# Performance work log

Hardware: AMD Instinct MI355X
Metric: run time of the kernel (lower is better)

## Reference

```python
import jax, jax.numpy as jnp
import numpy as np

# Module constants (from source defaults)
RING = 256      # ring_len
D = 128         # slot_dim
IN = 64         # input_dim
SD = max(8, D // 3)  # sensory_dim = 42
K = 2           # gauss_k -> 2K+1 = 5 taps
TAU = 8.0       # gauss_tau
NC = 1000       # num_classes
B, T = 512, 512


def setup_inputs() -> dict:
    key = jax.random.key(0)
    ks = jax.random.split(key, 10)
    g = lambda k, shape, s=0.05: jax.random.normal(k, shape, jnp.float32) * s
    return {
        "x": jax.random.normal(ks[0], (B, T, IN), jnp.float32),
        "theta_ptr": jnp.array([37.0], jnp.float32),
        "w_proj": g(ks[1], (SD, IN)), "b_proj": jnp.zeros((SD,), jnp.float32),
        "w_ih": g(ks[2], (3 * SD, SD)), "w_hh": g(ks[3], (3 * SD, SD)),
        "b_ih": jnp.zeros((3 * SD,), jnp.float32), "b_hh": jnp.zeros((3 * SD,), jnp.float32),
        "w_bridge": g(ks[4], (D, SD)), "b_bridge": jnp.zeros((D,), jnp.float32),
        "w_jump": g(ks[5], (1, D)), "b_jump": jnp.zeros((1,), jnp.float32),
        "w_gate": g(ks[6], (1, D)), "b_gate": jnp.zeros((1,), jnp.float32),
        "w_cls": g(ks[7], (NC, D)), "b_cls": jnp.zeros((NC,), jnp.float32),
    }


def _kernel(ptr):
    """Gaussian soft window around a fractional ring pointer. ptr: [B] float."""
    offs = jnp.arange(-K, K + 1)
    base = jnp.floor(ptr)
    frac = ptr - base                               # [B]
    pos = jnp.mod(base.astype(jnp.int32)[:, None] + offs[None, :], RING)  # [B, 2K+1]
    d = offs.astype(ptr.dtype)[None, :] - frac[:, None]
    w = jax.nn.softmax(-(d * d) / TAU, axis=-1)     # [B, 2K+1]
    return pos, w


def reference(x, theta_ptr, w_proj, b_proj, w_ih, w_hh, b_ih, b_hh,
              w_bridge, b_bridge, w_jump, b_jump, w_gate, b_gate, w_cls, b_cls):
    Bn = x.shape[0]
    bidx = jnp.arange(Bn)
    ring0 = jnp.zeros((Bn, RING, D), x.dtype)
    h0 = jnp.zeros((Bn, SD), x.dtype)
    ptr0 = jnp.broadcast_to(jnp.mod(theta_ptr, float(RING)), (Bn,)).astype(x.dtype)

    def step(carry, xt):
        ring, h, ptr = carry
        # sensory path: Linear -> GRUCell -> bridge
        s = xt @ w_proj.T + b_proj
        gx = s @ w_ih.T + b_ih
        gh = h @ w_hh.T + b_hh
        rg = jax.nn.sigmoid(gx[:, :SD] + gh[:, :SD])
        zg = jax.nn.sigmoid(gx[:, SD:2 * SD] + gh[:, SD:2 * SD])
        ng = jnp.tanh(gx[:, 2 * SD:] + rg * gh[:, 2 * SD:])
        h = (1.0 - zg) * ng + zg * h
        u = jnp.tanh(h @ w_bridge.T + b_bridge)      # write vector [B, D]
        # soft-kernel read at current pointer
        pos, w = _kernel(ptr)
        r = jnp.einsum('bk,bkd->bd', w, ring[bidx[:, None], pos])
        # pointer jump target + gate, circ_lerp along shortest arc
        jump = jax.nn.sigmoid(r @ w_jump.T + b_jump)[:, 0] * RING
        gate = jax.nn.sigmoid(r @ w_gate.T + b_gate)[:, 0]
        delta = jnp.mod(jump - ptr + RING / 2.0, float(RING)) - RING / 2.0  # wrap_delta
        ptr = jnp.mod(ptr + gate * delta, float(RING))                      # circ_lerp
        # soft-kernel write at new pointer
        pos2, w2 = _kernel(ptr)
        ring = ring.at[bidx[:, None], pos2].add(w2[..., None] * u[:, None, :])
        return (ring, h, ptr), None

    (ring, h, ptr), _ = jax.lax.scan(step, (ring0, h0, ptr0), jnp.swapaxes(x, 0, 1))
    pos, w = _kernel(ptr)
    r = jnp.einsum('bk,bkd->bd', w, ring[bidx[:, None], pos])
    return r @ w_cls.T + b_cls
```

## Files before the change

### kernel.cpp

```cpp
#include <hip/hip_runtime.h>
#include <hip/hip_bf16.h>
#include <cstdint>

#define RINGN 256
#define DD    128
#define SDN   42
#define G3N   126
#define INN   64
#define BN    512
#define TN    512
#define NCN   1000
#define HS    44
#define GXS   128
#define BT    (BN * TN)
#define HSLOTS 32

typedef float v2f __attribute__((ext_vector_type(2)));
typedef float4 __attribute__((may_alias)) f4ma;
typedef float2 __attribute__((may_alias)) f2ma;

__device__ __forceinline__ float sigm(float x)    { return 1.0f / (1.0f + __expf(-x)); }
__device__ __forceinline__ float tanhfast(float x){ float e = __expf(2.0f * x); return 1.0f - 2.0f / (e + 1.0f); }
__device__ __forceinline__ float wrap256(float x) { return x - 256.0f * floorf(x * 0.00390625f); }

__device__ __forceinline__ void taps_norm(float p, int* pos, float* w) {
  float base = floorf(p);
  float frac = p - base;
  int ib = (int)base;
  float e[5];
  float s = 0.0f;
#pragma unroll
  for (int k = 0; k < 5; k++) {
    float d = (float)(k - 2) - frac;
    e[k] = __expf(-(d * d) * 0.125f);
    s += e[k];
    pos[k] = (ib + k - 2) & 255;
  }
  float inv = 1.0f / s;
#pragma unroll
  for (int k = 0; k < 5; k++) w[k] = e[k] * inv;
}

template<int C>
__device__ __forceinline__ float dpp_add_step(float x) {
  int t = __builtin_amdgcn_update_dpp(0, __float_as_int(x), C, 0xf, 0xf, true);
  return x + __int_as_float(t);
}
__device__ __forceinline__ float wave_sum64(float x) {
  x = dpp_add_step<0x111>(x);
  x = dpp_add_step<0x112>(x);
  x = dpp_add_step<0x114>(x);
  x = dpp_add_step<0x118>(x);
  x = dpp_add_step<0x142>(x);
  x = dpp_add_step<0x143>(x);
  return __int_as_float(__builtin_amdgcn_readlane(__float_as_int(x), 63));
}

__global__ void prep_kernel(const float* __restrict__ w_ih, const float* __restrict__ w_proj,
                            const float* __restrict__ b_proj, const float* __restrict__ b_ih,
                            float* __restrict__ Wc, float* __restrict__ bc) {
  int idx = blockIdx.x * 256 + threadIdx.x;
  if (idx < G3N * INN) {
    int j = idx / INN, i = idx % INN;
    float a = 0.0f;
    for (int k = 0; k < SDN; k++) a += w_ih[j * SDN + k] * w_proj[k * INN + i];
    Wc[idx] = a;
  }
  if (idx < G3N) {
    float a = b_ih[idx];
    for (int k = 0; k < SDN; k++) a += w_ih[idx * SDN + k] * b_proj[k];
    bc[idx] = a;
  }
}

__global__ __launch_bounds__(256)
void gx_gemm(const float* __restrict__ x, const float* __restrict__ Wc,
             const float* __restrict__ bc, float* __restrict__ gxp) {
  __shared__ __align__(16) float WcS[G3N * INN];
  __shared__ float bcS[G3N + 2];
  __shared__ float tileS[256 * 33];
  const int tid = threadIdx.x;
  const float4* wc4 = (const float4*)Wc;
  float4* wcs4 = (float4*)WcS;
  for (int i = tid; i < G3N * INN / 4; i += 256) wcs4[i] = wc4[i];
  if (tid < G3N) bcS[tid] = bc[tid];
  __syncthreads();

  const size_t row0 = (size_t)blockIdx.x * 256;
  const size_t row = row0 + tid;
  v2f xr[INN / 2];
#pragma unroll
  for (int i = 0; i < INN / 4; i++) {
    float4 v = *reinterpret_cast<const float4*>(&x[row * INN + i * 4]);
    xr[2 * i]     = (v2f){v.x, v.y};
    xr[2 * i + 1] = (v2f){v.z, v.w};
  }

  for (int c0 = 0; c0 < GXS; c0 += 32) {
#pragma unroll
    for (int cc = 0; cc < 32; cc++) {
      int c = c0 + cc;
      float val = 0.0f;
      if (c < G3N) {
        const v2f* w = (const v2f*)&WcS[c * INN];
        v2f acc2 = (v2f){bcS[c], 0.0f};
#pragma unroll
        for (int i = 0; i < INN / 2; i++) acc2 = __builtin_elementwise_fma(w[i], xr[i], acc2);
        val = acc2.x + acc2.y;
      }
      tileS[tid * 33 + cc] = val;
    }
    __syncthreads();
#pragma unroll
    for (int i = 0; i < 8; i++) {
      int f = i * 256 + tid;
      int r = f >> 3;
      int cc4 = (f & 7) * 4;
      float4 v = make_float4(tileS[r * 33 + cc4], tileS[r * 33 + cc4 + 1],
                             tileS[r * 33 + cc4 + 2], tileS[r * 33 + cc4 + 3]);
      *reinterpret_cast<float4*>(&gxp[(row0 + r) * GXS + c0 + cc4]) = v;
    }
    __syncthreads();
  }
}

__global__ __launch_bounds__(192, 1)
void rec3_kernel(const float* __restrict__ gxp,
                 const float* __restrict__ w_hh, const float* __restrict__ b_hh,
                 const float* __restrict__ w_bridge, const float* __restrict__ b_bridge,
                 const float* __restrict__ w_jump, const float* __restrict__ b_jump,
                 const float* __restrict__ w_gate, const float* __restrict__ b_gate,
                 const float* __restrict__ theta,
                 float* __restrict__ hbuf, float* __restrict__ ptrbuf) {
  const int tid = threadIdx.x;
  const int wid = tid >> 6;
  const int lane = tid & 63;
  const int b = blockIdx.x;

  __shared__ float2 JG[RINGN];
  __shared__ __align__(16) float h_ring[HSLOTS * HS];
  __shared__ float ringJ[TN];
  __shared__ float ringG[TN];
  __shared__ int flagH;
  __shared__ int done1;

  if (tid == 0) { flagH = 0; done1 = 0; }
  __syncthreads();

  if (wid == 0) {
    const int jj = (lane < SDN) ? lane : (SDN - 1);

    const v2f* whh2 = (const v2f*)w_hh;
    v2f Whr[21], Whz[21], Whn[21];
#pragma unroll
    for (int k = 0; k < 21; k++) {
      Whr[k] = whh2[jj * 21 + k];
      Whz[k] = whh2[(jj + SDN) * 21 + k];
      Whn[k] = whh2[(jj + 2 * SDN) * 21 + k];
    }
    const float bhr = b_hh[jj], bhz = b_hh[jj + SDN], bhn = b_hh[jj + 2 * SDN];

    v2f hv2[22];
#pragma unroll
    for (int k = 0; k < 22; k++) hv2[k] = (v2f){0.f, 0.f};
    float hprev = 0.0f;

    const float* gxr = gxp + (size_t)b * TN * GXS;
    const int o0 = jj, o1 = SDN + jj, o2 = 2 * SDN + jj;
    float* hb = hbuf + (size_t)b * TN * HS;

    float pA0 = gxr[o0], pA1 = gxr[o1], pA2 = gxr[o2];
    float pB0 = gxr[GXS + o0], pB1 = gxr[GXS + o1], pB2 = gxr[GXS + o2];

    volatile int* fH = &flagH;
    volatile int* fC = &done1;

    auto STEP = [&](int t, float pgx0, float pgx1, float pgx2) {
      if ((t & 7) == 0 && t >= HSLOTS) {
        while (*fC < t - 24) __builtin_amdgcn_s_sleep(1);
      }
      v2f ar = (v2f){bhr, 0.f}, az = (v2f){bhz, 0.f}, an = (v2f){bhn, 0.f};
#pragma unroll
      for (int k = 0; k < 21; k++) {
        v2f h2 = hv2[k];
        ar = __builtin_elementwise_fma(Whr[k], h2, ar);
        az = __builtin_elementwise_fma(Whz[k], h2, az);
        an = __builtin_elementwise_fma(Whn[k], h2, an);
      }
      float ghr = ar.x + ar.y, ghz = az.x + az.y, ghn = an.x + an.y;
      float rgate = sigm(pgx0 + ghr);
      float zg = sigm(pgx1 + ghz);
      float ng = tanhfast(pgx2 + rgate * ghn);
      float hn = (1.0f - zg) * ng + zg * hprev;
      hprev = hn;

      float* slot = &h_ring[(t & (HSLOTS - 1)) * HS];
      if (lane < SDN) {
        slot[lane] = hn;
        hb[(size_t)t * HS + lane] = hn;
      }
      asm volatile("s_waitcnt lgkmcnt(0)" ::: "memory");
      if (lane == 0) *fH = t + 1;
      __builtin_amdgcn_wave_barrier();
      asm volatile("" ::: "memory");

#pragma unroll
      for (int i = 0; i < 11; i++) {
        float4 v = *(const f4ma*)(&slot[i * 4]);
        hv2[2 * i]     = (v2f){v.x, v.y};
        hv2[2 * i + 1] = (v2f){v.z, v.w};
      }
    };

    for (int t = 0; t < TN; t += 2) {
      STEP(t, pA0, pA1, pA2);
      if (t + 2 < TN) {
        const float* g = gxr + (size_t)(t + 2) * GXS;
        pA0 = g[o0]; pA1 = g[o1]; pA2 = g[o2];
      }
      STEP(t + 1, pB0, pB1, pB2);
      if (t + 3 < TN) {
        const float* g = gxr + (size_t)(t + 3) * GXS;
        pB0 = g[o0]; pB1 = g[o1]; pB2 = g[o2];
      }
    }
  } else if (wid == 1) {
    const int r1 = lane + 64;
    const v2f* wb2 = (const v2f*)w_bridge;
    v2f Wb0[21], Wb1[21];
#pragma unroll
    for (int k = 0; k < 21; k++) {
      Wb0[k] = wb2[lane * 21 + k];
      Wb1[k] = wb2[r1 * 21 + k];
    }
    const float bb0 = b_bridge[lane], bb1 = b_bridge[r1];
    const float wj0 = w_jump[lane], wj1 = w_jump[r1];
    const float wg0 = w_gate[lane], wg1 = w_gate[r1];

    volatile int* fH = &flagH;
    volatile int* fC = &done1;
    int seenH = 0;

    for (int t = 0; t < TN; t++) {
      if (seenH <= t) {
        while ((seenH = *fH) <= t) __builtin_amdgcn_s_sleep(1);
      }
      asm volatile("" ::: "memory");
      const float* slot = &h_ring[(t & (HSLOTS - 1)) * HS];
      v2f hw[22];
#pragma unroll
      for (int i = 0; i < 11; i++) {
        float4 v = *(const f4ma*)(&slot[i * 4]);
        hw[2 * i]     = (v2f){v.x, v.y};
        hw[2 * i + 1] = (v2f){v.z, v.w};
      }
      v2f a0 = (v2f){bb0, 0.f}, a1 = (v2f){bb1, 0.f};
#pragma unroll
      for (int k = 0; k < 21; k++) {
        v2f h2 = hw[k];
        a0 = __builtin_elementwise_fma(Wb0[k], h2, a0);
        a1 = __builtin_elementwise_fma(Wb1[k], h2, a1);
      }
      float u0 = tanhfast(a0.x + a0.y);
      float u1 = tanhfast(a1.x + a1.y);

      float pjs = wave_sum64(u0 * wj0 + u1 * wj1);
      float pgs = wave_sum64(u0 * wg0 + u1 * wg1);

      if (lane == 0) { ringJ[t] = pjs; ringG[t] = pgs; }
      asm volatile("s_waitcnt lgkmcnt(0)" ::: "memory");
      if (lane == 0) *fC = t + 1;
    }
  } else {
    for (int i = lane; i < RINGN; i += 64) JG[i] = make_float2(0.f, 0.f);
    __builtin_amdgcn_wave_barrier();
    asm volatile("" ::: "memory");

    const float bj = b_jump[0], bg = b_gate[0];
    float ptr = wrap256(theta[0]);
    float* pb = ptrbuf + (size_t)b * TN;

    float wk[5]; float2 Vk[5];
    {
      int posk[5];
      taps_norm(ptr, posk, wk);
#pragma unroll
      for (int k = 0; k < 5; k++) Vk[k] = JG[posk[k]];
    }
    float pjprev = 0.f, pgprev = 0.f, S2prev = 0.f;
    volatile int* rdy = &done1;
    int seen = 0;

    for (int t = 0; t < TN; t++) {
      float dotJ = 0.f, dotG = 0.f;
#pragma unroll
      for (int k = 0; k < 5; k++) { dotJ += wk[k] * Vk[k].x; dotG += wk[k] * Vk[k].y; }
      float Jv = fmaf(pjprev, S2prev, dotJ);
      float Gv = fmaf(pgprev, S2prev, dotG);
      float jump = 256.0f * sigm(Jv + bj);
      float gate = sigm(Gv + bg);
      float delta = wrap256(jump - ptr + 128.0f) - 128.0f;
      float ptr2 = wrap256(ptr + gate * delta);

      float tbase = floorf(ptr2);
      float frac = ptr2 - tbase;
      int ib = (int)tbase;
      float e2[5], ssum = 0.f; int pos2[5];
#pragma unroll
      for (int k = 0; k < 5; k++) {
        float d = (float)(k - 2) - frac;
        e2[k] = __expf(-(d * d) * 0.125f);
        ssum += e2[k];
        pos2[k] = (ib + k - 2) & 255;
      }
      float inv2 = 1.0f / ssum;
      float2 Vk2[5];
#pragma unroll
      for (int k = 0; k < 5; k++) Vk2[k] = JG[pos2[k]];
      float w2n[5], S2 = 0.f;
#pragma unroll
      for (int k = 0; k < 5; k++) { w2n[k] = e2[k] * inv2; S2 = fmaf(w2n[k], w2n[k], S2); }
      if (lane == 0) pb[t] = ptr2;

      if (seen <= t) {
        while ((seen = *rdy) <= t) __builtin_amdgcn_s_sleep(1);
      }
      asm volatile("" ::: "memory");
      float pjs = ringJ[t];
      float pgs = ringG[t];

      int p2sel = pos2[0]; float w2sel = w2n[0];
#pragma unroll
      for (int k = 1; k < 5; k++) {
        if (lane == k) { p2sel = pos2[k]; w2sel = w2n[k]; }
      }
      if (lane < 5) {
        atomicAdd(&JG[p2sel].x, w2sel * pjs);
        atomicAdd(&JG[p2sel].y, w2sel * pgs);
      }

#pragma unroll
      for (int k = 0; k < 5; k++) { wk[k] = w2n[k]; Vk[k] = Vk2[k]; }
      S2prev = S2; pjprev = pjs; pgprev = pgs; ptr = ptr2;
    }
  }
}

__global__ __launch_bounds__(64)
void rfinal_kernel(const float* __restrict__ hbuf, const float* __restrict__ ptrbuf,
                   const float* __restrict__ w_bridge, const float* __restrict__ b_bridge,
                   float* __restrict__ rbuf) {
  const int b = blockIdx.x;
  const int chunk = blockIdx.y;
  const int lane = threadIdx.x;
  const int t0 = chunk * 128;
  const int r1 = lane + 64;

  __shared__ float c_lds[128];

  const float* pb = ptrbuf + (size_t)b * TN;
  float ptrf = pb[TN - 1];
  int posf[5]; float wf[5];
  taps_norm(ptrf, posf, wf);

#pragma unroll
  for (int rr = 0; rr < 2; rr++) {
    int tt = rr * 64 + lane;
    int p2[5]; float w2[5];
    taps_norm(pb[t0 + tt], p2, w2);
    float c = 0.0f;
#pragma unroll
    for (int k = 0; k < 5; k++)
#pragma unroll
      for (int k2 = 0; k2 < 5; k2++)
        c += (posf[k] == p2[k2]) ? wf[k] * w2[k2] : 0.0f;
    c_lds[tt] = c;
  }
  __builtin_amdgcn_wave_barrier();
  asm volatile("" ::: "memory");

  const v2f* wb2 = (const v2f*)w_bridge;
  v2f Wb0[21], Wb1[21];
#pragma unroll
  for (int k = 0; k < 21; k++) { Wb0[k] = wb2[lane * 21 + k]; Wb1[k] = wb2[r1 * 21 + k]; }
  float bb0 = b_bridge[lane], bb1 = b_bridge[r1];

  float racc0 = 0.0f, racc1 = 0.0f;
  for (int tt = 0; tt < 128; tt++) {
    float ct = c_lds[tt];
    if (ct != 0.0f) {
      const f4ma* hp = (const f4ma*)(hbuf + ((size_t)b * TN + t0 + tt) * HS);
      v2f hx[22];
#pragma unroll
      for (int i = 0; i < 11; i++) {
        float4 v = hp[i];
        hx[2 * i]     = (v2f){v.x, v.y};
        hx[2 * i + 1] = (v2f){v.z, v.w};
      }
      v2f a0 = (v2f){bb0, 0.f}, a1 = (v2f){bb1, 0.f};
#pragma unroll
      for (int k = 0; k < 21; k++) {
        a0 = __builtin_elementwise_fma(Wb0[k], hx[k], a0);
        a1 = __builtin_elementwise_fma(Wb1[k], hx[k], a1);
      }
      racc0 += ct * tanhfast(a0.x + a0.y);
      racc1 += ct * tanhfast(a1.x + a1.y);
    }
  }
  atomicAdd(&rbuf[b * DD + lane], racc0);
  atomicAdd(&rbuf[b * DD + 64 + lane], racc1);
}

__global__ __launch_bounds__(256)
void cls_kernel(const float* __restrict__ rbuf, const float* __restrict__ w_cls,
                const float* __restrict__ b_cls, float* __restrict__ out) {
  const int b0 = blockIdx.x * 4;
  const int tid = threadIdx.x;
  __shared__ __align__(16) float r[4 * DD];
  for (int i = tid; i < 4 * DD; i += 256) r[i] = rbuf[(size_t)b0 * DD + i];
  __syncthreads();

  for (int c = tid; c < NCN; c += 256) {
    float bcv = b_cls[c];
    float a0 = bcv, a1 = bcv, a2 = bcv, a3 = bcv;
    const float* wrow = &w_cls[(size_t)c * DD];
#pragma unroll
    for (int d4 = 0; d4 < DD / 4; d4++) {
      float4 wv = *reinterpret_cast<const float4*>(&wrow[d4 * 4]);
      float4 r0 = *(const f4ma*)(&r[0 * DD + d4 * 4]);
      float4 r1 = *(const f4ma*)(&r[1 * DD + d4 * 4]);
      float4 r2 = *(const f4ma*)(&r[2 * DD + d4 * 4]);
      float4 r3 = *(const f4ma*)(&r[3 * DD + d4 * 4]);
      a0 += wv.x * r0.x + wv.y * r0.y + wv.z * r0.z + wv.w * r0.w;
      a1 += wv.x * r1.x + wv.y * r1.y + wv.z * r1.z + wv.w * r1.w;
      a2 += wv.x * r2.x + wv.y * r2.y + wv.z * r2.z + wv.w * r2.w;
      a3 += wv.x * r3.x + wv.y * r3.y + wv.z * r3.z + wv.w * r3.w;
    }
    out[(size_t)(b0 + 0) * NCN + c] = a0;
    out[(size_t)(b0 + 1) * NCN + c] = a1;
    out[(size_t)(b0 + 2) * NCN + c] = a2;
    out[(size_t)(b0 + 3) * NCN + c] = a3;
  }
}

extern "C" void kernel_launch(void* const* d_in, const int* in_sizes, int n_in,
                              void* d_out, int out_size, void* d_ws, size_t ws_size,
                              hipStream_t stream) {
  const float* x        = (const float*)d_in[0];
  const float* theta    = (const float*)d_in[1];
  const float* w_proj   = (const float*)d_in[2];
  const float* b_proj   = (const float*)d_in[3];
  const float* w_ih     = (const float*)d_in[4];
  const float* w_hh     = (const float*)d_in[5];
  const float* b_ih     = (const float*)d_in[6];
  const float* b_hh     = (const float*)d_in[7];
  const float* w_bridge = (const float*)d_in[8];
  const float* b_bridge = (const float*)d_in[9];
  const float* w_jump   = (const float*)d_in[10];
  const float* b_jump   = (const float*)d_in[11];
  const float* w_gate   = (const float*)d_in[12];
  const float* b_gate   = (const float*)d_in[13];
  const float* w_cls    = (const float*)d_in[14];
  const float* b_cls    = (const float*)d_in[15];
  float* out = (float*)d_out;

  char* ws = (char*)d_ws;
  size_t off = 0;
  float* gxp    = (float*)(ws + off); off += (size_t)BT * GXS * 4;
  float* hbuf   = (float*)(ws + off); off += (size_t)BN * TN * HS * 4;
  float* ptrbuf = (float*)(ws + off); off += (size_t)BN * TN * 4;
  float* rbuf   = (float*)(ws + off); off += (size_t)BN * DD * 4;
  float* Wc     = (float*)(ws + off); off += (((size_t)G3N * INN * 4 + 255) & ~(size_t)255);
  float* bc     = (float*)(ws + off); off += 512;

  hipMemsetAsync(rbuf, 0, (size_t)BN * DD * 4, stream);
  prep_kernel<<<32, 256, 0, stream>>>(w_ih, w_proj, b_proj, b_ih, Wc, bc);
  gx_gemm<<<BT / 256, 256, 0, stream>>>(x, Wc, bc, gxp);
  rec3_kernel<<<BN, 192, 0, stream>>>(gxp, w_hh, b_hh, w_bridge, b_bridge,
                                      w_jump, b_jump, w_gate, b_gate, theta, hbuf, ptrbuf);
  dim3 gfin(BN, 4);
  rfinal_kernel<<<gfin, 4 * 16, 0, stream>>>(hbuf, ptrbuf, w_bridge, b_bridge, rbuf);
  cls_kernel<<<BN / 4, 256, 0, stream>>>(rbuf, w_cls, b_cls, out);
}
```

Before: 543.4 us.

## Fuse input-gate GEMM into recurrent kernel via producer wave and LDS ring

```diff
diff --git a/kernel.cpp b/kernel.cpp
--- a/kernel.cpp
+++ b/kernel.cpp
@@ -14,6 +14,7 @@
 #define GXS   128
 #define BT    (BN * TN)
 #define HSLOTS 32
+#define GSLOTS 16
 
 typedef float v2f __attribute__((ext_vector_type(2)));
 typedef float4 __attribute__((may_alias)) f4ma;
@@ -73,59 +74,10 @@
   }
 }
 
-__global__ __launch_bounds__(256)
-void gx_gemm(const float* __restrict__ x, const float* __restrict__ Wc,
-             const float* __restrict__ bc, float* __restrict__ gxp) {
-  __shared__ __align__(16) float WcS[G3N * INN];
-  __shared__ float bcS[G3N + 2];
-  __shared__ float tileS[256 * 33];
-  const int tid = threadIdx.x;
-  const float4* wc4 = (const float4*)Wc;
-  float4* wcs4 = (float4*)WcS;
-  for (int i = tid; i < G3N * INN / 4; i += 256) wcs4[i] = wc4[i];
-  if (tid < G3N) bcS[tid] = bc[tid];
-  __syncthreads();
-
-  const size_t row0 = (size_t)blockIdx.x * 256;
-  const size_t row = row0 + tid;
-  v2f xr[INN / 2];
-#pragma unroll
-  for (int i = 0; i < INN / 4; i++) {
-    float4 v = *reinterpret_cast<const float4*>(&x[row * INN + i * 4]);
-    xr[2 * i]     = (v2f){v.x, v.y};
-    xr[2 * i + 1] = (v2f){v.z, v.w};
-  }
-
-  for (int c0 = 0; c0 < GXS; c0 += 32) {
-#pragma unroll
-    for (int cc = 0; cc < 32; cc++) {
-      int c = c0 + cc;
-      float val = 0.0f;
-      if (c < G3N) {
-        const v2f* w = (const v2f*)&WcS[c * INN];
-        v2f acc2 = (v2f){bcS[c], 0.0f};
-#pragma unroll
-        for (int i = 0; i < INN / 2; i++) acc2 = __builtin_elementwise_fma(w[i], xr[i], acc2);
-        val = acc2.x + acc2.y;
-      }
-      tileS[tid * 33 + cc] = val;
-    }
-    __syncthreads();
-#pragma unroll
-    for (int i = 0; i < 8; i++) {
-      int f = i * 256 + tid;
-      int r = f >> 3;
-      int cc4 = (f & 7) * 4;
-      float4 v = make_float4(tileS[r * 33 + cc4], tileS[r * 33 + cc4 + 1],
-                             tileS[r * 33 + cc4 + 2], tileS[r * 33 + cc4 + 3]);
-      *reinterpret_cast<float4*>(&gxp[(row0 + r) * GXS + c0 + cc4]) = v;
-    }
-    __syncthreads();
-  }
-}
-
-__global__ __launch_bounds__(192, 1)
-void rec3_kernel(const float* __restrict__ gxp,
+__global__ __launch_bounds__(256, 1)
+void rec4_kernel(const float* __restrict__ x,
+                 const float* __restrict__ Wc,
+                 const float* __restrict__ bc,
                  const float* __restrict__ w_hh, const float* __restrict__ b_hh,
                  const float* __restrict__ w_bridge, const float* __restrict__ b_bridge,
                  const float* __restrict__ w_jump, const float* __restrict__ b_jump,
@@ -139,15 +91,62 @@
 
   __shared__ float2 JG[RINGN];
   __shared__ __align__(16) float h_ring[HSLOTS * HS];
+  __shared__ __align__(16) float gx_ring[GSLOTS * GXS];
+  __shared__ __align__(16) float xst[2 * INN];
   __shared__ float ringJ[TN];
   __shared__ float ringG[TN];
   __shared__ int flagH;
   __shared__ int done1;
-
-  if (tid == 0) { flagH = 0; done1 = 0; }
+  __shared__ int flagG;
+
+  if (tid == 0) { flagH = 0; done1 = 0; flagG = 0; }
   __syncthreads();
 
-  if (wid == 0) {
+  if (wid == 3) {
+    const v2f* wc2 = (const v2f*)Wc;
+    v2f Wr0[32], Wr1[32];
+#pragma unroll
+    for (int i = 0; i < 32; i++) {
+      Wr0[i] = wc2[lane * 32 + i];
+      Wr1[i] = (lane < 62) ? wc2[(64 + lane) * 32 + i] : (v2f){0.f, 0.f};
+    }
+    const float bcv0 = bc[lane];
+    const float bcv1 = (lane < 62) ? bc[64 + lane] : 0.0f;
+
+    const float* xb = x + (size_t)b * TN * INN;
+    float xcur = xb[lane];
+    float xnxt = xb[INN + lane];
+
+    volatile int* fH = &flagH;
+    volatile int* fG = &flagG;
+
+    for (int t = 0; t < TN; t++) {
+      if (t >= 12) {
+        while (*fH < t - 12) __builtin_amdgcn_s_sleep(1);
+      }
+      float* xs = &xst[(t & 1) * INN];
+      xs[lane] = xcur;
+      __builtin_amdgcn_wave_barrier();
+      asm volatile("" ::: "memory");
+      const f2ma* xp = (const f2ma*)xs;
+      v2f acc0 = (v2f){bcv0, 0.0f};
+      v2f acc1 = (v2f){bcv1, 0.0f};
+#pragma unroll
+      for (int i = 0; i < 32; i++) {
+        float2 xv = xp[i];
+        v2f xr = (v2f){xv.x, xv.y};
+        acc0 = __builtin_elementwise_fma(Wr0[i], xr, acc0);
+        acc1 = __builtin_elementwise_fma(Wr1[i], xr, acc1);
+      }
+      float* slot = &gx_ring[(t & (GSLOTS - 1)) * GXS];
+      slot[lane] = acc0.x + acc0.y;
+      if (lane < 62) slot[64 + lane] = acc1.x + acc1.y;
+      asm volatile("s_waitcnt lgkmcnt(0)" ::: "memory");
+      if (lane == 0) *fG = t + 1;
+      xcur = xnxt;
+      if (t + 2 < TN) xnxt = xb[(size_t)(t + 2) * INN + lane];
+    }
+  } else if (wid == 0) {
     const int jj = (lane < SDN) ? lane : (SDN - 1);
 
     const v2f* whh2 = (const v2f*)w_hh;
@@ -165,17 +164,19 @@
     for (int k = 0; k < 22; k++) hv2[k] = (v2f){0.f, 0.f};
     float hprev = 0.0f;
 
-    const float* gxr = gxp + (size_t)b * TN * GXS;
     const int o0 = jj, o1 = SDN + jj, o2 = 2 * SDN + jj;
     float* hb = hbuf + (size_t)b * TN * HS;
 
-    float pA0 = gxr[o0], pA1 = gxr[o1], pA2 = gxr[o2];
-    float pB0 = gxr[GXS + o0], pB1 = gxr[GXS + o1], pB2 = gxr[GXS + o2];
-
     volatile int* fH = &flagH;
     volatile int* fC = &done1;
-
-    auto STEP = [&](int t, float pgx0, float pgx1, float pgx2) {
+    volatile int* fG = &flagG;
+    int seenG = 0;
+
+    if (seenG < 1) { while ((seenG = *fG) < 1) __builtin_amdgcn_s_sleep(1); }
+    asm volatile("" ::: "memory");
+    float cu0 = gx_ring[o0], cu1 = gx_ring[o1], cu2 = gx_ring[o2];
+
+    for (int t = 0; t < TN; t++) {
       if ((t & 7) == 0 && t >= HSLOTS) {
         while (*fC < t - 24) __builtin_amdgcn_s_sleep(1);
       }
@@ -188,9 +189,9 @@
         an = __builtin_elementwise_fma(Whn[k], h2, an);
       }
       float ghr = ar.x + ar.y, ghz = az.x + az.y, ghn = an.x + an.y;
-      float rgate = sigm(pgx0 + ghr);
-      float zg = sigm(pgx1 + ghz);
-      float ng = tanhfast(pgx2 + rgate * ghn);
+      float rgate = sigm(cu0 + ghr);
+      float zg = sigm(cu1 + ghz);
+      float ng = tanhfast(cu2 + rgate * ghn);
       float hn = (1.0f - zg) * ng + zg * hprev;
       hprev = hn;
 
@@ -205,23 +206,19 @@
       asm volatile("" ::: "memory");
 
 #pragma unroll
-      for (int i = 0; i < 11; i++) {
-        float4 v = *(const f4ma*)(&slot[i * 4]);
-        hv2[2 * i]     = (v2f){v.x, v.y};
-        hv2[2 * i + 1] = (v2f){v.z, v.w};
-      }
-    };
-
-    for (int t = 0; t < TN; t += 2) {
-      STEP(t, pA0, pA1, pA2);
-      if (t + 2 < TN) {
-        const float* g = gxr + (size_t)(t + 2) * GXS;
-        pA0 = g[o0]; pA1 = g[o1]; pA2 = g[o2];
-      }
-      STEP(t + 1, pB0, pB1, pB2);
-      if (t + 3 < TN) {
-        const float* g = gxr + (size_t)(t + 3) * GXS;
-        pB0 = g[o0]; pB1 = g[o1]; pB2 = g[o2];
+      for (int k4 = 0; k4 < 11; k4++) {
+        float4 v = *(const f4ma*)(&slot[k4 * 4]);
+        hv2[2 * k4]     = (v2f){v.x, v.y};
+        hv2[2 * k4 + 1] = (v2f){v.z, v.w};
+      }
+
+      if (t + 1 < TN) {
+        if (seenG < t + 2) {
+          while ((seenG = *fG) < t + 2) __builtin_amdgcn_s_sleep(1);
+        }
+        asm volatile("" ::: "memory");
+        const float* gs = &gx_ring[((t + 1) & (GSLOTS - 1)) * GXS];
+        cu0 = gs[o0]; cu1 = gs[o1]; cu2 = gs[o2];
       }
     }
   } else if (wid == 1) {
@@ -249,10 +246,10 @@
       const float* slot = &h_ring[(t & (HSLOTS - 1)) * HS];
       v2f hw[22];
 #pragma unroll
-      for (int i = 0; i < 11; i++) {
-        float4 v = *(const f4ma*)(&slot[i * 4]);
-        hw[2 * i]     = (v2f){v.x, v.y};
-        hw[2 * i + 1] = (v2f){v.z, v.w};
+      for (int k4 = 0; k4 < 11; k4++) {
+        float4 v = *(const f4ma*)(&slot[k4 * 4]);
+        hw[2 * k4]     = (v2f){v.x, v.y};
+        hw[2 * k4 + 1] = (v2f){v.z, v.w};
       }
       v2f a0 = (v2f){bb0, 0.f}, a1 = (v2f){bb1, 0.f};
 #pragma unroll
@@ -466,7 +463,6 @@
 
   char* ws = (char*)d_ws;
   size_t off = 0;
-  float* gxp    = (float*)(ws + off); off += (size_t)BT * GXS * 4;
   float* hbuf   = (float*)(ws + off); off += (size_t)BN * TN * HS * 4;
   float* ptrbuf = (float*)(ws + off); off += (size_t)BN * TN * 4;
   float* rbuf   = (float*)(ws + off); off += (size_t)BN * DD * 4;
@@ -475,10 +471,9 @@
 
   hipMemsetAsync(rbuf, 0, (size_t)BN * DD * 4, stream);
   prep_kernel<<<32, 256, 0, stream>>>(w_ih, w_proj, b_proj, b_ih, Wc, bc);
-  gx_gemm<<<BT / 256, 256, 0, stream>>>(x, Wc, bc, gxp);
-  rec3_kernel<<<BN, 192, 0, stream>>>(gxp, w_hh, b_hh, w_bridge, b_bridge,
+  rec4_kernel<<<BN, 256, 0, stream>>>(x, Wc, bc, w_hh, b_hh, w_bridge, b_bridge,
                                       w_jump, b_jump, w_gate, b_gate, theta, hbuf, ptrbuf);
   dim3 gfin(BN, 4);
-  rfinal_kernel<<<gfin, 4 * 16, 0, stream>>>(hbuf, ptrbuf, w_bridge, b_bridge, rbuf);
+  rfinal_kernel<<<gfin, 64, 0, stream>>>(hbuf, ptrbuf, w_bridge, b_bridge, rbuf);
   cls_kernel<<<BN / 4, 256, 0, stream>>>(rbuf, w_cls, b_cls, out);
 }
```

New measurement: 563.1 us. 3.6% more time.
